# Kernel optimization log

Hardware: AMD Instinct MI355X
Metric: run time of the kernel (lower is better)

Reference implementation:

```python
import jax, jax.numpy as jnp
import numpy as np

N_EMBD = 1024
N_HEAD = 16
B, L = 4, 2048


def setup_inputs() -> dict:
    key = jax.random.key(0)
    ks = jax.random.split(key, 5)
    scale = 1.0 / np.sqrt(N_EMBD)
    x = jax.random.normal(ks[0], (B, L, N_EMBD), dtype=jnp.float32)
    # nn.Linear(n_embd, n_embd, bias=False) weights, stored torch-style (out, in)
    Wq = jax.random.uniform(ks[1], (N_EMBD, N_EMBD), jnp.float32, -scale, scale)
    Wk = jax.random.uniform(ks[2], (N_EMBD, N_EMBD), jnp.float32, -scale, scale)
    Wv = jax.random.uniform(ks[3], (N_EMBD, N_EMBD), jnp.float32, -scale, scale)
    Wp = jax.random.uniform(ks[4], (N_EMBD, N_EMBD), jnp.float32, -scale, scale)
    attn_mask = jnp.ones((B, L), dtype=jnp.int32)
    return {"x": x, "Wq": Wq, "Wk": Wk, "Wv": Wv, "Wp": Wp, "attn_mask": attn_mask}


def reference(x, Wq, Wk, Wv, Wp, attn_mask):
    Bq, Lq, C = x.shape
    hd = C // N_HEAD
    # torch Linear: y = x @ W.T
    def split_heads(y):
        return y.reshape(Bq, Lq, N_HEAD, hd).transpose(0, 2, 1, 3)  # (B,H,L,hd)
    q = split_heads(x @ Wq.T)
    k = split_heads(x @ Wk.T)
    v = split_heads(x @ Wv.T)
    att = jnp.einsum("bhqd,bhkd->bhqk", q, k) / np.sqrt(hd)  # (B,H,L,L)
    causal = jnp.tril(jnp.ones((Lq, Lq), dtype=bool))
    neg_inf = jnp.float32(-jnp.inf)
    att = jnp.where(causal[None, None, :, :], att, neg_inf)
    pad = (attn_mask != 0)[:, None, None, :]  # (B,1,1,L) key-side padding mask
    att = jnp.where(pad, att, neg_inf)
    att = jax.nn.softmax(att, axis=-1)
    y = jnp.einsum("bhqk,bhkd->bhqd", att, v)
    y = y.transpose(0, 2, 1, 3).reshape(Bq, Lq, C)
    return y @ Wp.T
```

## Files before the change

### kernel.cpp

```cpp
#include <hip/hip_runtime.h>

typedef __attribute__((ext_vector_type(8))) short short8;
typedef __attribute__((ext_vector_type(4))) float floatx4;

#define CEMB 1024
#define NHEAD 16
#define HD 64
#define BATCH 4
#define SEQ 2048

#define BARRIER() asm volatile("s_waitcnt lgkmcnt(0)\n\ts_barrier" ::: "memory")

__device__ __forceinline__ unsigned short f2bf(float f) {
    union { float f; unsigned int i; } x; x.f = f;
    unsigned int r = x.i + 0x7FFFu + ((x.i >> 16) & 1u);
    return (unsigned short)(r >> 16);
}
__device__ __forceinline__ unsigned int packbf_trunc(float a, float b) {
    union { float f; unsigned int u; } x, y; x.f = a; y.f = b;
    return (x.u >> 16) | (y.u & 0xFFFF0000u);
}

#define GLD16(gp, lp) \
    __builtin_amdgcn_global_load_lds((const __attribute__((address_space(1))) void*)(gp), \
                                     (__attribute__((address_space(3))) void*)(lp), 16, 0, 0)

__global__ void cast_x(const float* __restrict__ src, unsigned short* __restrict__ dst, int n4) {
    int i = blockIdx.x * blockDim.x + threadIdx.x;
    if (i < n4) {
        float4 v = ((const float4*)src)[i];
        ushort4 o;
        o.x = f2bf(v.x); o.y = f2bf(v.y); o.z = f2bf(v.z); o.w = f2bf(v.w);
        ((ushort4*)dst)[i] = o;
    }
}

__global__ void cast_w(const float* __restrict__ w0, const float* __restrict__ w1,
                       const float* __restrict__ w2, const float* __restrict__ w3,
                       unsigned short* __restrict__ o0, unsigned short* __restrict__ o1,
                       unsigned short* __restrict__ o2, unsigned short* __restrict__ o3) {
    int which = blockIdx.y;
    const float* src = which == 0 ? w0 : which == 1 ? w1 : which == 2 ? w2 : w3;
    unsigned short* dst = which == 0 ? o0 : which == 1 ? o1 : which == 2 ? o2 : o3;
    float scale = (which == 0) ? 0.125f * 1.44269504088896f : 1.0f;
    int i = blockIdx.x * blockDim.x + threadIdx.x;
    float4 v = ((const float4*)src)[i];
    ushort4 o;
    o.x = f2bf(v.x * scale); o.y = f2bf(v.y * scale);
    o.z = f2bf(v.z * scale); o.w = f2bf(v.w * scale);
    ((ushort4*)dst)[i] = o;
}


#define MFMA __builtin_amdgcn_mfma_f32_16x16x32_bf16

#define STAGE(Ab, Bb, k0) do {                                                  \
    GLD16(aS + (k0),             (Ab) + aLS);                                   \
    GLD16(aS + (k0) + 64 * CEMB, (Ab) + aLS + 2048);                            \
    GLD16(bS + (k0),             (Bb) + aLS);                                   \
    GLD16(bS + (k0) + 64 * CEMB, (Bb) + aLS + 2048);                            \
} while (0)

#define TILE(t, drain, do_stage) do {                                           \
    unsigned short* Ab = &As[(t) & 1][0];                                       \
    unsigned short* Bb = &Bs[(t) & 1][0];                                       \
    if (drain) { asm volatile("s_waitcnt vmcnt(0)" ::: "memory"); }             \
    else       { asm volatile("s_waitcnt vmcnt(4)" ::: "memory"); }             \
    asm volatile("s_barrier" ::: "memory");                                     \
    short8 af[4], bfr[4];                                                       \
    _Pragma("unroll")                                                           \
    for (int mm = 0; mm < 4; ++mm)                                              \
        af[mm] = *(const short8*)((Ab) + aOffR + mm * 512 + ck);                \
    _Pragma("unroll")                                                           \
    for (int nn = 0; nn < 2; ++nn)                                              \
        bfr[nn] = *(const short8*)((Bb) + bOffR + nn * 512 + ck);               \
    __builtin_amdgcn_s_setprio(1);                                              \
    _Pragma("unroll")                                                           \
    for (int mm = 0; mm < 4; ++mm)                                              \
        _Pragma("unroll")                                                       \
        for (int nn = 0; nn < 2; ++nn)                                          \
            acc[mm][nn] = MFMA(af[mm], bfr[nn], acc[mm][nn], 0, 0, 0);          \
    __builtin_amdgcn_s_setprio(0);                                              \
    __builtin_amdgcn_sched_barrier(0);                                          \
    _Pragma("unroll")                                                           \
    for (int nn = 2; nn < 4; ++nn)                                              \
        bfr[nn] = *(const short8*)((Bb) + bOffR + nn * 512 + ck);               \
    asm volatile("s_waitcnt lgkmcnt(0)\n\ts_barrier" ::: "memory");             \
    __builtin_amdgcn_sched_barrier(0);                                          \
    if (do_stage) STAGE(Ab, Bb, ((t) + 2) * 32);                                \
    __builtin_amdgcn_s_setprio(1);                                              \
    _Pragma("unroll")                                                           \
    for (int mm = 0; mm < 4; ++mm)                                              \
        _Pragma("unroll")                                                       \
        for (int nn = 2; nn < 4; ++nn)                                          \
            acc[mm][nn] = MFMA(af[mm], bfr[nn], acc[mm][nn], 0, 0, 0);          \
    __builtin_amdgcn_s_setprio(0);                                              \
    __builtin_amdgcn_sched_barrier(0);                                          \
} while (0)

__launch_bounds__(256, 4)
__global__ void gemm_128(const unsigned short* __restrict__ A,
                         const unsigned short* __restrict__ W,
                         void* __restrict__ O0, void* __restrict__ O1,
                         void* __restrict__ O2, int mode, int ntn) {
    __shared__ unsigned short As[2][4096];
    __shared__ unsigned short Bs[2][4096];

    int nwg = gridDim.x;
    int bid = blockIdx.x;
    int wg = (bid & 7) * (nwg >> 3) + (bid >> 3);
    int cpr = ntn >> 2;
    int c = wg >> 5, r = wg & 31;
    int cm = c / cpr, cn = c - cm * cpr;
    int mt = cm * 8 + (r >> 2);
    int nt = cn * 4 + (r & 3);
    int m0 = mt * 128, n0 = nt * 128;

    int tid = threadIdx.x;
    int wave = tid >> 6, lane = tid & 63;
    int l16 = lane & 15, quad = lane >> 4;
    int wm = wave >> 1, wn = wave & 1;

    int r0 = tid >> 2;
    int p0 = tid & 3;
    int cl = (p0 ^ (r0 & 3)) * 8;
    const unsigned short* aS = A + (size_t)(m0 + r0) * CEMB + cl;
    const unsigned short* bS = W + (size_t)(n0 + r0) * CEMB + cl;
    int aLS = wave * 512;

    int aOffR = (wm * 64 + l16) * 32;
    int bOffR = (wn * 64 + l16) * 32;
    int ck = (quad ^ (l16 & 3)) * 8;

    floatx4 acc[4][4];
    #pragma unroll
    for (int mm = 0; mm < 4; ++mm)
        #pragma unroll
        for (int nn = 0; nn < 4; ++nn) acc[mm][nn] = (floatx4){0.f, 0.f, 0.f, 0.f};

    STAGE(&As[0][0], &Bs[0][0], 0);
    STAGE(&As[1][0], &Bs[1][0], 32);

    #pragma unroll 2
    for (int t = 0; t < 30; ++t) { TILE(t, false, true); }
    TILE(30, false, false);
    TILE(31, true, false);

    if (mode == 1) {
        float* Of = (float*)O0;
        #pragma unroll
        for (int mf = 0; mf < 4; ++mf)
            #pragma unroll
            for (int j = 0; j < 4; ++j) {
                int m = m0 + wm * 64 + mf * 16 + quad * 4 + j;
                #pragma unroll
                for (int nf = 0; nf < 4; ++nf) {
                    int n = n0 + wn * 64 + nf * 16 + l16;
                    Of[(size_t)m * CEMB + n] = acc[mf][nf][j];
                }
            }
    } else {
        int which = n0 >> 10;
        unsigned short* out = (unsigned short*)(which == 0 ? O0 : which == 1 ? O1 : O2);
        if (which < 2) {
            #pragma unroll
            for (int mf = 0; mf < 4; ++mf)
                #pragma unroll
                for (int j = 0; j < 4; ++j) {
                    int m = m0 + wm * 64 + mf * 16 + quad * 4 + j;
                    int bb = m >> 11, ll = m & (SEQ - 1);
                    #pragma unroll
                    for (int nf = 0; nf < 4; ++nf) {
                        int n = (n0 & (CEMB - 1)) + wn * 64 + nf * 16 + l16;
                        int h = n >> 6, d = n & (HD - 1);
                        out[(size_t)((bb * NHEAD + h) * SEQ + ll) * HD + d] =
                            f2bf(acc[mf][nf][j]);
                    }
                }
        } else {
            #pragma unroll
            for (int mf = 0; mf < 4; ++mf) {
                int m = m0 + wm * 64 + mf * 16 + quad * 4;
                int bb = m >> 11, ll = m & (SEQ - 1);
                #pragma unroll
                for (int nf = 0; nf < 4; ++nf) {
                    int n = (n0 & (CEMB - 1)) + wn * 64 + nf * 16 + l16;
                    int h = n >> 6, d = n & (HD - 1);
                    ushort4 o4;
                    o4.x = f2bf(acc[mf][nf][0]); o4.y = f2bf(acc[mf][nf][1]);
                    o4.z = f2bf(acc[mf][nf][2]); o4.w = f2bf(acc[mf][nf][3]);
                    *(ushort4*)&out[(size_t)((bb * NHEAD + h) * HD + d) * SEQ + ll] = o4;
                }
            }
        }
    }
}

__launch_bounds__(256, 2)
__global__ void attn_mfma(const unsigned short* __restrict__ Qb,
                          const unsigned short* __restrict__ Kb,
                          const unsigned short* __restrict__ Vtg,
                          const int* __restrict__ amask,
                          unsigned short* __restrict__ Yb) {
    __shared__ unsigned short Ks[64 * 64];
    __shared__ unsigned short Vs[64 * 64];
    __shared__ unsigned short Ps[128 * 64];

    int tid = threadIdx.x;
    int wave = tid >> 6;
    int lane = tid & 63;
    int l16 = lane & 15;
    int quad = lane >> 4;
    int l7 = l16 & 7;

    int n = blockIdx.x;
    int rr = n >> 8;
    int i = n & 255;
    int base = i & 15;
    int bh = (i >> 4) + (rr << 4);
    int qt = (rr == 0) ? base
           : (rr == 1) ? 15 - base
           : (rr == 2) ? (base ^ 8)
                       : 15 - (base ^ 8);

    int bidx = bh >> 4;
    int h = bh & (NHEAD - 1);
    size_t hbase = (size_t)bh * SEQ * HD;

    int r0 = tid >> 3, p0 = tid & 7;
    int cl = p0 ^ (r0 & 7);
    unsigned short* kDst0 = Ks + r0 * 64 + p0 * 8;
    unsigned short* kDst1 = kDst0 + 32 * 64;
    unsigned short* vDst0 = Vs + r0 * 64 + p0 * 8;
    unsigned short* vDst1 = vDst0 + 32 * 64;
    const unsigned short* kSrc0 = Kb + hbase + (size_t)r0 * HD + cl * 8;
    const unsigned short* kSrc1 = kSrc0 + (size_t)32 * HD;
    const unsigned short* vSrc0 = Vtg + hbase + (size_t)r0 * SEQ + cl * 8;
    const unsigned short* vSrc1 = vSrc0 + (size_t)32 * SEQ;
    const int* mSrc = amask + bidx * SEQ + quad * 4;

    int q0 = qt * 128;
    int nkt = 2 * qt + 2;

    short8 qf[2][2];
    #pragma unroll
    for (int qsub = 0; qsub < 2; ++qsub)
        #pragma unroll
        for (int kk = 0; kk < 2; ++kk)
            qf[qsub][kk] = *(const short8*)(Qb + hbase +
                (size_t)(q0 + wave * 32 + qsub * 16 + l16) * HD + kk * 32 + quad * 8);

    short8 kr0 = *(const short8*)(kSrc0);
    short8 kr1 = *(const short8*)(kSrc1);
    short8 vr0 = *(const short8*)(vSrc0);
    short8 vr1 = *(const short8*)(vSrc1);
    int4 cmi[4];
    #pragma unroll
    for (int t = 0; t < 4; ++t) cmi[t] = *(const int4*)(mSrc + t * 16);

    floatx4 o[2][4];
    #pragma unroll
    for (int qsub = 0; qsub < 2; ++qsub)
        #pragma unroll
        for (int t = 0; t < 4; ++t) o[qsub][t] = (floatx4){0.f, 0.f, 0.f, 0.f};
    float ls[2] = {0.f, 0.f};

    int qw = q0 + wave * 32;

    for (int jt = 0; jt < nkt; ++jt) {
        BARRIER();
        *(short8*)kDst0 = kr0;
        *(short8*)kDst1 = kr1;
        *(short8*)vDst0 = vr0;
        *(short8*)vDst1 = vr1;
        int4 cm[4];
        #pragma unroll
        for (int t = 0; t < 4; ++t) cm[t] = cmi[t];
        if (jt + 1 < nkt) {
            size_t ko = (size_t)(jt + 1) * 64;
            kr0 = *(const short8*)(kSrc0 + ko * HD);
            kr1 = *(const short8*)(kSrc1 + ko * HD);
            vr0 = *(const short8*)(vSrc0 + ko);
            vr1 = *(const short8*)(vSrc1 + ko);
            #pragma unroll
            for (int t = 0; t < 4; ++t) cmi[t] = *(const int4*)(mSrc + (jt + 1) * 64 + t * 16);
        }
        BARRIER();

        if (jt * 64 <= qw + 31) {
            floatx4 sc[2][4];
            #pragma unroll
            for (int qsub = 0; qsub < 2; ++qsub)
                #pragma unroll
                for (int t = 0; t < 4; ++t) sc[qsub][t] = (floatx4){0.f, 0.f, 0.f, 0.f};
            __builtin_amdgcn_s_setprio(1);
            #pragma unroll
            for (int kk = 0; kk < 2; ++kk)
                #pragma unroll
                for (int t = 0; t < 4; ++t) {
                    short8 aK = *(const short8*)(Ks + (t * 16 + l16) * 64 +
                                                 ((kk * 4 + quad) ^ l7) * 8);
                    #pragma unroll
                    for (int qsub = 0; qsub < 2; ++qsub)
                        sc[qsub][t] = __builtin_amdgcn_mfma_f32_16x16x32_bf16(
                            aK, qf[qsub][kk], sc[qsub][t], 0, 0, 0);
                }
            __builtin_amdgcn_s_setprio(0);

            bool needc = (jt * 64 + 63 > qw);

            #pragma unroll
            for (int qsub = 0; qsub < 2; ++qsub) {
                int qi = q0 + wave * 32 + qsub * 16 + l16;
                #pragma unroll
                for (int t = 0; t < 4; ++t) {
                    int kb = jt * 64 + t * 16 + quad * 4;
                    float p[4];
                    #pragma unroll
                    for (int j = 0; j < 4; ++j) {
                        float sv = sc[qsub][t][j];
                        if (needc) sv = (kb + j <= qi) ? sv : -1e30f;
                        sv = cm[t][j] ? sv : -1e30f;
                        p[j] = __builtin_amdgcn_exp2f(sv);
                        ls[qsub] += p[j];
                    }
                    int row = wave * 32 + qsub * 16 + l16;
                    int pos = (t * 2 + (quad >> 1)) ^ l7;
                    uint2 pk;
                    pk.x = packbf_trunc(p[0], p[1]);
                    pk.y = packbf_trunc(p[2], p[3]);
                    *(uint2*)(Ps + row * 64 + pos * 8 + (quad & 1) * 4) = pk;
                }
            }

            __builtin_amdgcn_s_setprio(1);
            #pragma unroll
            for (int kk = 0; kk < 2; ++kk) {
                short8 pa[2];
                #pragma unroll
                for (int qsub = 0; qsub < 2; ++qsub)
                    pa[qsub] = *(const short8*)(Ps + (wave * 32 + qsub * 16 + l16) * 64 +
                                                ((kk * 4 + quad) ^ l7) * 8);
                #pragma unroll
                for (int t = 0; t < 4; ++t) {
                    short8 vb = *(const short8*)(Vs + (t * 16 + l16) * 64 +
                                                 ((kk * 4 + quad) ^ l7) * 8);
                    #pragma unroll
                    for (int qsub = 0; qsub < 2; ++qsub)
                        o[qsub][t] = __builtin_amdgcn_mfma_f32_16x16x32_bf16(
                            pa[qsub], vb, o[qsub][t], 0, 0, 0);
                }
            }
            __builtin_amdgcn_s_setprio(0);
        }
    }

    #pragma unroll
    for (int qsub = 0; qsub < 2; ++qsub) {
        ls[qsub] += __shfl_xor(ls[qsub], 16, 64);
        ls[qsub] += __shfl_xor(ls[qsub], 32, 64);
    }

    #pragma unroll
    for (int qsub = 0; qsub < 2; ++qsub)
        #pragma unroll
        for (int j = 0; j < 4; ++j) {
            float lq = __shfl(ls[qsub], quad * 4 + j, 64);
            float inv = 1.0f / lq;
            size_t row = (size_t)bidx * SEQ + q0 + wave * 32 + qsub * 16 + quad * 4 + j;
            #pragma unroll
            for (int t = 0; t < 4; ++t)
                Yb[row * CEMB + h * HD + t * 16 + l16] = f2bf(o[qsub][t][j] * inv);
        }
}

extern "C" void kernel_launch(void* const* d_in, const int* in_sizes, int n_in,
                              void* d_out, int out_size, void* d_ws, size_t ws_size,
                              hipStream_t stream) {
    const float* x  = (const float*)d_in[0];
    const float* Wq = (const float*)d_in[1];
    const float* Wk = (const float*)d_in[2];
    const float* Wv = (const float*)d_in[3];
    const float* Wp = (const float*)d_in[4];
    const int* amask = (const int*)d_in[5];

    char* ws = (char*)d_ws;
    unsigned short* xb  = (unsigned short*)(ws + 0);
    unsigned short* Wqb = (unsigned short*)(ws + (16u << 20));
    unsigned short* Wkb = (unsigned short*)(ws + (18u << 20));
    unsigned short* Wvb = (unsigned short*)(ws + (20u << 20));
    unsigned short* Wpb = (unsigned short*)(ws + (22u << 20));
    unsigned short* Qb  = (unsigned short*)(ws + (24u << 20));
    unsigned short* Kb  = (unsigned short*)(ws + (40u << 20));
    unsigned short* Vtg = (unsigned short*)(ws + (56u << 20));
    unsigned short* Yb  = (unsigned short*)(ws + (72u << 20));

    const int NX4 = (BATCH * SEQ * CEMB) / 4;
    const int NW4 = (CEMB * CEMB) / 4;
    cast_x<<<dim3(NX4 / 256), 256, 0, stream>>>(x, xb, NX4);
    cast_w<<<dim3(NW4 / 256, 4), 256, 0, stream>>>(Wq, Wk, Wv, Wp, Wqb, Wkb, Wvb, Wpb);

    gemm_128<<<dim3(1536), 256, 0, stream>>>(
        xb, Wqb, (void*)Qb, (void*)Kb, (void*)Vtg, 0, 24);

    attn_mfma<<<dim3(1024), 256, 0, stream>>>(Qb, Kb, Vtg, amask, Yb);

    gemm_128<<<dim3(512), 256, 0, stream>>>(
        Yb, Wpb, d_out, nullptr, nullptr, 1, 8);
}
```

Baseline: 294.8 us.

## Deepen GEMM LDS pipeline to four stages and drop attention setprio

The projection GEMM moves from double-buffered to quad-buffered LDS staging, prefetching four k-tiles ahead with tapering vmcnt waits at the tail, and the occupancy hint drops from 4 to 2 to fit the larger shared-memory footprint. The aim is to hide more global-load latency behind MFMA work. Separately, the s_setprio bumps around the MFMA blocks in the attention kernel are removed. The trade-off is fewer resident workgroups per CU in the GEMM, which gives less latency hiding across waves.

```diff
diff --git a/kernel.cpp b/kernel.cpp
--- a/kernel.cpp
+++ b/kernel.cpp
@@ -55,17 +55,16 @@
 #define MFMA __builtin_amdgcn_mfma_f32_16x16x32_bf16
 
 #define STAGE(Ab, Bb, k0) do {                                                  \
-    GLD16(aS + (k0),             (Ab) + aLS);                                   \
-    GLD16(aS + (k0) + 64 * CEMB, (Ab) + aLS + 2048);                            \
-    GLD16(bS + (k0),             (Bb) + aLS);                                   \
-    GLD16(bS + (k0) + 64 * CEMB, (Bb) + aLS + 2048);                            \
+    GLD16(aS + (size_t)(k0),             (Ab) + aLS);                           \
+    GLD16(aS + (size_t)(k0) + 64 * CEMB, (Ab) + aLS + 2048);                    \
+    GLD16(bS + (size_t)(k0),             (Bb) + aLS);                           \
+    GLD16(bS + (size_t)(k0) + 64 * CEMB, (Bb) + aLS + 2048);                    \
 } while (0)
 
-#define TILE(t, drain, do_stage) do {                                           \
-    unsigned short* Ab = &As[(t) & 1][0];                                       \
-    unsigned short* Bb = &Bs[(t) & 1][0];                                       \
-    if (drain) { asm volatile("s_waitcnt vmcnt(0)" ::: "memory"); }             \
-    else       { asm volatile("s_waitcnt vmcnt(4)" ::: "memory"); }             \
+#define TILE(t, VMN, do_stage) do {                                             \
+    unsigned short* Ab = &As[(t) & 3][0];                                       \
+    unsigned short* Bb = &Bs[(t) & 3][0];                                       \
+    asm volatile("s_waitcnt vmcnt(" #VMN ")" ::: "memory");                     \
     asm volatile("s_barrier" ::: "memory");                                     \
     short8 af[4], bfr[4];                                                       \
     _Pragma("unroll")                                                           \
@@ -87,7 +86,7 @@
         bfr[nn] = *(const short8*)((Bb) + bOffR + nn * 512 + ck);               \
     asm volatile("s_waitcnt lgkmcnt(0)\n\ts_barrier" ::: "memory");             \
     __builtin_amdgcn_sched_barrier(0);                                          \
-    if (do_stage) STAGE(Ab, Bb, ((t) + 2) * 32);                                \
+    if (do_stage) STAGE(Ab, Bb, ((t) + 4) * 32);                                \
     __builtin_amdgcn_s_setprio(1);                                              \
     _Pragma("unroll")                                                           \
     for (int mm = 0; mm < 4; ++mm)                                              \
@@ -98,13 +97,13 @@
     __builtin_amdgcn_sched_barrier(0);                                          \
 } while (0)
 
-__launch_bounds__(256, 4)
+__launch_bounds__(256, 2)
 __global__ void gemm_128(const unsigned short* __restrict__ A,
                          const unsigned short* __restrict__ W,
                          void* __restrict__ O0, void* __restrict__ O1,
                          void* __restrict__ O2, int mode, int ntn) {
-    __shared__ unsigned short As[2][4096];
-    __shared__ unsigned short Bs[2][4096];
+    __shared__ unsigned short As[4][4096];
+    __shared__ unsigned short Bs[4][4096];
 
     int nwg = gridDim.x;
     int bid = blockIdx.x;
@@ -140,11 +139,20 @@
 
     STAGE(&As[0][0], &Bs[0][0], 0);
     STAGE(&As[1][0], &Bs[1][0], 32);
-
-    #pragma unroll 2
-    for (int t = 0; t < 30; ++t) { TILE(t, false, true); }
-    TILE(30, false, false);
-    TILE(31, true, false);
+    STAGE(&As[2][0], &Bs[2][0], 64);
+    STAGE(&As[3][0], &Bs[3][0], 96);
+
+    for (int tt = 0; tt < 7; ++tt) {
+        int t = 4 * tt;
+        TILE(t + 0, 12, true);
+        TILE(t + 1, 12, true);
+        TILE(t + 2, 12, true);
+        TILE(t + 3, 12, true);
+    }
+    TILE(28, 12, false);
+    TILE(29, 8, false);
+    TILE(30, 4, false);
+    TILE(31, 0, false);
 
     if (mode == 1) {
         float* Of = (float*)O0;
@@ -293,7 +301,6 @@
             for (int qsub = 0; qsub < 2; ++qsub)
                 #pragma unroll
                 for (int t = 0; t < 4; ++t) sc[qsub][t] = (floatx4){0.f, 0.f, 0.f, 0.f};
-            __builtin_amdgcn_s_setprio(1);
             #pragma unroll
             for (int kk = 0; kk < 2; ++kk)
                 #pragma unroll
@@ -305,7 +312,6 @@
                         sc[qsub][t] = __builtin_amdgcn_mfma_f32_16x16x32_bf16(
                             aK, qf[qsub][kk], sc[qsub][t], 0, 0, 0);
                 }
-            __builtin_amdgcn_s_setprio(0);
 
             bool needc = (jt * 64 + 63 > qw);
 
@@ -333,7 +339,6 @@
                 }
             }
 
-            __builtin_amdgcn_s_setprio(1);
             #pragma unroll
             for (int kk = 0; kk < 2; ++kk) {
                 short8 pa[2];
@@ -351,7 +356,6 @@
                             pa[qsub], vb, o[qsub][t], 0, 0, 0);
                 }
             }
-            __builtin_amdgcn_s_setprio(0);
         }
     }
 
```

New measurement: 255.7 us. -13.3%, faster.
